# Kernel tuning notes

Hardware: AMD Instinct MI355X
Metric: run time of the kernel (lower is better)

## Reference

```python
import jax, jax.numpy as jnp
import numpy as np

EPS = 1e-5  # BatchNorm1d default eps


def setup_inputs() -> dict:
    key = jax.random.key(0)
    k1, k2 = jax.random.split(key)
    b, d, h, w = 32, 256, 32, 128
    x = jax.random.normal(k1, (b, d, h, w), dtype=jnp.float32)
    # mask=True means padded/masked position (excluded from stats, left untouched)
    mask = jax.random.randint(k2, (b, 1, h, w), 0, 2).astype(bool)
    gamma = jnp.ones((d,), dtype=jnp.float32)
    beta = jnp.zeros((d,), dtype=jnp.float32)
    return {"x": x, "mask": mask, "gamma": gamma, "beta": beta}


def reference(x, mask, gamma, beta):
    # x: [b, d, h, w], mask: [b, 1, h, w] (True = masked)
    not_mask = ~mask[:, 0]                      # [b, h, w]
    wgt = not_mask.astype(x.dtype)              # [b, h, w]
    count = jnp.maximum(wgt.sum(), jnp.asarray(1.0, x.dtype))
    xt = jnp.transpose(x, (0, 2, 3, 1))         # [b, h, w, d]
    wm = wgt[..., None]                         # [b, h, w, 1]
    # masked per-channel batch statistics (biased variance, as BN training mode)
    mean = (xt * wm).sum(axis=(0, 1, 2)) / count                  # [d]
    var = (wm * (xt - mean) ** 2).sum(axis=(0, 1, 2)) / count     # [d]
    normed = (xt - mean) * jax.lax.rsqrt(var + EPS) * gamma + beta
    out = jnp.where(not_mask[..., None], normed, xt)              # scatter-back
    return jnp.transpose(out, (0, 3, 1, 2))     # [b, d, h, w]
```

## Files before the change

### kernel.cpp

```cpp
#include <hip/hip_runtime.h>

#define BB 32
#define DD 256
#define HW 4096
#define DHW (DD * HW)
#define EPS 1e-5f

typedef float floatx4 __attribute__((ext_vector_type(4)));

__global__ void __launch_bounds__(1024, 4)
channel_kernel(const float* __restrict__ x, const int* __restrict__ mask,
               const float* __restrict__ gamma, const float* __restrict__ beta,
               float* __restrict__ out) {
    const int d = blockIdx.x;
    const int tid = threadIdx.x;
    const int wave = tid >> 6, lane = tid & 63;

    const float4* __restrict__ xv4 = reinterpret_cast<const float4*>(x);
    const int4*   __restrict__ mv4 = reinterpret_cast<const int4*>(mask);
    const int xbase = d * 1024 + tid;

    float sum = 0.f, sq = 0.f, cnt = 0.f;
#pragma unroll 1
    for (int g = 0; g < 4; ++g) {
        float4 xs[8];
        int4   ms[8];
#pragma unroll
        for (int k = 0; k < 8; ++k) {
            const int b = g * 8 + k;
            xs[k] = xv4[b * (DHW / 4) + xbase];
            ms[k] = mv4[b * 1024 + tid];
        }
#pragma unroll
        for (int k = 0; k < 8; ++k) {
            const float vx = ms[k].x ? 0.f : xs[k].x;
            const float vy = ms[k].y ? 0.f : xs[k].y;
            const float vz = ms[k].z ? 0.f : xs[k].z;
            const float vw = ms[k].w ? 0.f : xs[k].w;
            sum += vx + vy + vz + vw;
            sq  += vx * vx + vy * vy + vz * vz + vw * vw;
            cnt += (ms[k].x ? 0.f : 1.f) + (ms[k].y ? 0.f : 1.f)
                 + (ms[k].z ? 0.f : 1.f) + (ms[k].w ? 0.f : 1.f);
        }
    }

    __shared__ float rsum[16], rsq[16], rcnt[16];
    __shared__ float s_scale, s_bias;
#pragma unroll
    for (int off = 32; off > 0; off >>= 1) {
        sum += __shfl_down(sum, off);
        sq  += __shfl_down(sq, off);
        cnt += __shfl_down(cnt, off);
    }
    if (lane == 0) { rsum[wave] = sum; rsq[wave] = sq; rcnt[wave] = cnt; }
    __syncthreads();
    if (tid < 16) {
        float ts = rsum[tid], tq = rsq[tid], tc = rcnt[tid];
#pragma unroll
        for (int off = 8; off > 0; off >>= 1) {
            ts += __shfl_down(ts, off, 16);
            tq += __shfl_down(tq, off, 16);
            tc += __shfl_down(tc, off, 16);
        }
        if (tid == 0) {
            tc = fmaxf(tc, 1.0f);
            const float mean = ts / tc;
            const float var = fmaxf(tq / tc - mean * mean, 0.0f);
            const float sc = rsqrtf(var + EPS) * gamma[d];
            s_scale = sc;
            s_bias = beta[d] - mean * sc;
        }
    }
    __syncthreads();
    const float sc = s_scale, bi = s_bias;

    floatx4* __restrict__ ov4 = reinterpret_cast<floatx4*>(out);
#pragma unroll 1
    for (int g = 0; g < 4; ++g) {
        float4 xs[8];
        int4   ms[8];
#pragma unroll
        for (int k = 0; k < 8; ++k) {
            const int b = g * 8 + k;
            xs[k] = xv4[b * (DHW / 4) + xbase];
            ms[k] = mv4[b * 1024 + tid];
        }
#pragma unroll
        for (int k = 0; k < 8; ++k) {
            const int b = g * 8 + k;
            floatx4 o;
            o.x = ms[k].x ? xs[k].x : xs[k].x * sc + bi;
            o.y = ms[k].y ? xs[k].y : xs[k].y * sc + bi;
            o.z = ms[k].z ? xs[k].z : xs[k].z * sc + bi;
            o.w = ms[k].w ? xs[k].w : xs[k].w * sc + bi;
            __builtin_nontemporal_store(o, &ov4[b * (DHW / 4) + xbase]);
        }
    }
}

extern "C" void kernel_launch(void* const* d_in, const int* in_sizes, int n_in,
                              void* d_out, int out_size, void* d_ws, size_t ws_size,
                              hipStream_t stream) {
    const float* x     = (const float*)d_in[0];
    const int*   mask  = (const int*)d_in[1];
    const float* gamma = (const float*)d_in[2];
    const float* beta  = (const float*)d_in[3];
    float* out = (float*)d_out;

    channel_kernel<<<DD, 1024, 0, stream>>>(x, mask, gamma, beta, out);
}
```

Baseline: 65.54 us.

## Split each channel across four blocks with global-memory stat exchange and spin barrier

Each channel is now handled by four 256-thread blocks, each covering eight batch entries, instead of one 1024-thread block. Partial sums go to a workspace and a per-channel atomic counter (zeroed by a memset before launch) acts as a spin barrier, so every block can compute the final scale and bias. The goal is more, smaller blocks for better distribution across CUs and more latency hiding. The cost is an extra memset launch, global atomics and spin-waiting. The spin also assumes all four sibling blocks are resident at the same time, or it can deadlock.

```diff
diff --git a/kernel.cpp b/kernel.cpp
--- a/kernel.cpp
+++ b/kernel.cpp
@@ -6,45 +6,54 @@
 #define DHW (DD * HW)
 #define EPS 1e-5f
 
+#define SIB 4
+#define BPB (BB / SIB)
+#define NBLK (DD * SIB)
+
+#define WS_CTR_BYTE 16384
+
 typedef float floatx4 __attribute__((ext_vector_type(4)));
 
-__global__ void __launch_bounds__(1024, 4)
+__global__ void __launch_bounds__(256, 8)
 channel_kernel(const float* __restrict__ x, const int* __restrict__ mask,
                const float* __restrict__ gamma, const float* __restrict__ beta,
-               float* __restrict__ out) {
-    const int d = blockIdx.x;
+               float* __restrict__ ws, float* __restrict__ out) {
+    const int bid = blockIdx.x;
+    const int d = bid >> 2;
+    const int g = bid & 3;
+    const int b0 = g * BPB;
     const int tid = threadIdx.x;
     const int wave = tid >> 6, lane = tid & 63;
 
     const float4* __restrict__ xv4 = reinterpret_cast<const float4*>(x);
     const int4*   __restrict__ mv4 = reinterpret_cast<const int4*>(mask);
-    const int xbase = d * 1024 + tid;
+    const int sbase = d * 1024 + tid;
 
     float sum = 0.f, sq = 0.f, cnt = 0.f;
 #pragma unroll 1
-    for (int g = 0; g < 4; ++g) {
-        float4 xs[8];
-        int4   ms[8];
+    for (int bb = 0; bb < BPB; ++bb) {
+        const int b = b0 + bb;
+        float4 xs[4];
+        int4   ms[4];
 #pragma unroll
-        for (int k = 0; k < 8; ++k) {
-            const int b = g * 8 + k;
-            xs[k] = xv4[b * (DHW / 4) + xbase];
-            ms[k] = mv4[b * 1024 + tid];
+        for (int j = 0; j < 4; ++j) {
+            xs[j] = xv4[b * (DHW / 4) + sbase + j * 256];
+            ms[j] = mv4[b * 1024 + j * 256 + tid];
         }
 #pragma unroll
-        for (int k = 0; k < 8; ++k) {
-            const float vx = ms[k].x ? 0.f : xs[k].x;
-            const float vy = ms[k].y ? 0.f : xs[k].y;
-            const float vz = ms[k].z ? 0.f : xs[k].z;
-            const float vw = ms[k].w ? 0.f : xs[k].w;
+        for (int j = 0; j < 4; ++j) {
+            const float vx = ms[j].x ? 0.f : xs[j].x;
+            const float vy = ms[j].y ? 0.f : xs[j].y;
+            const float vz = ms[j].z ? 0.f : xs[j].z;
+            const float vw = ms[j].w ? 0.f : xs[j].w;
             sum += vx + vy + vz + vw;
             sq  += vx * vx + vy * vy + vz * vz + vw * vw;
-            cnt += (ms[k].x ? 0.f : 1.f) + (ms[k].y ? 0.f : 1.f)
-                 + (ms[k].z ? 0.f : 1.f) + (ms[k].w ? 0.f : 1.f);
+            cnt += (ms[j].x ? 0.f : 1.f) + (ms[j].y ? 0.f : 1.f)
+                 + (ms[j].z ? 0.f : 1.f) + (ms[j].w ? 0.f : 1.f);
         }
     }
 
-    __shared__ float rsum[16], rsq[16], rcnt[16];
+    __shared__ float rsum[4], rsq[4], rcnt[4];
     __shared__ float s_scale, s_bias;
 #pragma unroll
     for (int off = 32; off > 0; off >>= 1) {
@@ -54,46 +63,59 @@
     }
     if (lane == 0) { rsum[wave] = sum; rsq[wave] = sq; rcnt[wave] = cnt; }
     __syncthreads();
-    if (tid < 16) {
-        float ts = rsum[tid], tq = rsq[tid], tc = rcnt[tid];
+
+    unsigned* ctr = reinterpret_cast<unsigned*>(
+        reinterpret_cast<char*>(ws) + WS_CTR_BYTE) + d;
+    if (tid == 0) {
+        float ts = rsum[0] + rsum[1] + rsum[2] + rsum[3];
+        float tq = rsq[0] + rsq[1] + rsq[2] + rsq[3];
+        float tc = rcnt[0] + rcnt[1] + rcnt[2] + rcnt[3];
+        ws[bid * 4 + 0] = ts;
+        ws[bid * 4 + 1] = tq;
+        ws[bid * 4 + 2] = tc;
+        __threadfence();
+        __hip_atomic_fetch_add(ctr, 1u, __ATOMIC_RELEASE, __HIP_MEMORY_SCOPE_AGENT);
+        while (__hip_atomic_load(ctr, __ATOMIC_ACQUIRE, __HIP_MEMORY_SCOPE_AGENT)
+               < (unsigned)SIB) {
+            __builtin_amdgcn_s_sleep(1);
+        }
+        float fs = 0.f, fq = 0.f, fc = 0.f;
 #pragma unroll
-        for (int off = 8; off > 0; off >>= 1) {
-            ts += __shfl_down(ts, off, 16);
-            tq += __shfl_down(tq, off, 16);
-            tc += __shfl_down(tc, off, 16);
+        for (int s = 0; s < SIB; ++s) {
+            const int sb = (d * SIB + s) * 4;
+            fs += __hip_atomic_load(&ws[sb + 0], __ATOMIC_RELAXED, __HIP_MEMORY_SCOPE_AGENT);
+            fq += __hip_atomic_load(&ws[sb + 1], __ATOMIC_RELAXED, __HIP_MEMORY_SCOPE_AGENT);
+            fc += __hip_atomic_load(&ws[sb + 2], __ATOMIC_RELAXED, __HIP_MEMORY_SCOPE_AGENT);
         }
-        if (tid == 0) {
-            tc = fmaxf(tc, 1.0f);
-            const float mean = ts / tc;
-            const float var = fmaxf(tq / tc - mean * mean, 0.0f);
-            const float sc = rsqrtf(var + EPS) * gamma[d];
-            s_scale = sc;
-            s_bias = beta[d] - mean * sc;
-        }
+        fc = fmaxf(fc, 1.0f);
+        const float mean = fs / fc;
+        const float var = fmaxf(fq / fc - mean * mean, 0.0f);
+        const float sc = rsqrtf(var + EPS) * gamma[d];
+        s_scale = sc;
+        s_bias = beta[d] - mean * sc;
     }
     __syncthreads();
     const float sc = s_scale, bi = s_bias;
 
     floatx4* __restrict__ ov4 = reinterpret_cast<floatx4*>(out);
 #pragma unroll 1
-    for (int g = 0; g < 4; ++g) {
-        float4 xs[8];
-        int4   ms[8];
+    for (int bb = 0; bb < BPB; ++bb) {
+        const int b = b0 + bb;
+        float4 xs[4];
+        int4   ms[4];
 #pragma unroll
-        for (int k = 0; k < 8; ++k) {
-            const int b = g * 8 + k;
-            xs[k] = xv4[b * (DHW / 4) + xbase];
-            ms[k] = mv4[b * 1024 + tid];
+        for (int j = 0; j < 4; ++j) {
+            xs[j] = xv4[b * (DHW / 4) + sbase + j * 256];
+            ms[j] = mv4[b * 1024 + j * 256 + tid];
         }
 #pragma unroll
-        for (int k = 0; k < 8; ++k) {
-            const int b = g * 8 + k;
+        for (int j = 0; j < 4; ++j) {
             floatx4 o;
-            o.x = ms[k].x ? xs[k].x : xs[k].x * sc + bi;
-            o.y = ms[k].y ? xs[k].y : xs[k].y * sc + bi;
-            o.z = ms[k].z ? xs[k].z : xs[k].z * sc + bi;
-            o.w = ms[k].w ? xs[k].w : xs[k].w * sc + bi;
-            __builtin_nontemporal_store(o, &ov4[b * (DHW / 4) + xbase]);
+            o.x = ms[j].x ? xs[j].x : xs[j].x * sc + bi;
+            o.y = ms[j].y ? xs[j].y : xs[j].y * sc + bi;
+            o.z = ms[j].z ? xs[j].z : xs[j].z * sc + bi;
+            o.w = ms[j].w ? xs[j].w : xs[j].w * sc + bi;
+            __builtin_nontemporal_store(o, &ov4[b * (DHW / 4) + sbase + j * 256]);
         }
     }
 }
@@ -106,6 +128,8 @@
     const float* gamma = (const float*)d_in[2];
     const float* beta  = (const float*)d_in[3];
     float* out = (float*)d_out;
+    float* ws  = (float*)d_ws;
 
-    channel_kernel<<<DD, 1024, 0, stream>>>(x, mask, gamma, beta, out);
+    hipMemsetAsync((char*)d_ws + WS_CTR_BYTE, 0, DD * sizeof(unsigned), stream);
+    channel_kernel<<<NBLK, 256, 0, stream>>>(x, mask, gamma, beta, ws, out);
 }
```

After: 151.7 us. +131.4%, slower.
